# Performance work log

Hardware: AMD Instinct MI355X
Metric: run time of the kernel (lower is better)

## Reference

```python
import jax, jax.numpy as jnp
import numpy as np

VJ = 80                      # number of joints (groups)
DIMS = [480, 512, 256, 128, 64, 6]  # per-joint channel sizes through the 5 grouped 1x1 convs
RFF_K = 240                  # random fourier features -> 2*K = 480 channels
BATCH = 2048


def setup_inputs() -> dict:
    key = jax.random.key(0)
    ks = jax.random.split(key, 4 + 3 * 5)
    inp = {
        "querypoint": jax.random.normal(ks[0], (BATCH, VJ, 3), jnp.float32),
        "point_features": jax.random.normal(ks[1], (BATCH, VJ, DIMS[0]), jnp.float32),
        "adjmat": jax.random.uniform(ks[2], (VJ, VJ), jnp.float32),
        "Brff": jax.random.normal(ks[3], (3, RFF_K), jnp.float32),  # RandomFourierFeatEnc buffer (std=1)
    }
    ki = 4
    for i in range(5):
        cin, cout = DIMS[i], DIMS[i + 1]
        # weight_norm params: direction v [K, out, in], magnitude g [K, out], bias b [K, out]
        inp[f"v{i}"] = jax.random.normal(ks[ki], (VJ, cout, cin), jnp.float32) * 0.05; ki += 1
        inp[f"g{i}"] = jax.random.uniform(ks[ki], (VJ, cout), jnp.float32) + 0.5; ki += 1
        inp[f"b{i}"] = jax.random.normal(ks[ki], (VJ, cout), jnp.float32) * 0.01; ki += 1
    return inp


def _gconv(x, v, g, b):
    # grouped Conv1d(kernel=1, groups=VJ) == per-joint linear; weight_norm over per-output-channel fan-in
    w = v * (g / jnp.linalg.norm(v, axis=-1))[..., None]   # [K, out, in]
    return jnp.einsum('bki,koi->bko', x, w) + b            # [B, K, out]


def _leaky(x):
    return jnp.where(x >= 0, x, 0.01 * x)  # nn.LeakyReLU default slope


def reference(querypoint, point_features, adjmat, Brff,
              v0, g0, b0, v1, g1, b1, v2, g2, b2, v3, g3, b3, v4, g4, b4):
    # RandomFourierFeatEnc: cat(cos(2*pi*x@B), sin(2*pi*x@B))
    emb = 2.0 * jnp.pi * jnp.einsum('bnd,dk->bnk', querypoint, Brff)
    qf = jnp.concatenate([jnp.cos(emb), jnp.sin(emb)], axis=-1)   # [B, VJ, 480]
    h = point_features + qf
    # einsum 'bkjl,kk->bkjl' == scale each joint k by relu(adjmat)[k,k] (diagonal extraction)
    scale = jax.nn.relu(jnp.diagonal(adjmat))[None, :, None]      # [1, VJ, 1]
    h = _leaky(_gconv(h, v0, g0, b0)) * scale
    h = _leaky(_gconv(h, v1, g1, b1)) * scale
    h = _leaky(_gconv(h, v2, g2, b2)) * scale
    h = _leaky(_gconv(h, v3, g3, b3))
    return _gconv(h, v4, g4, b4)                                  # [B, VJ, 6]
```

## Files before the change

kernel.cpp:

```cpp
#include <hip/hip_runtime.h>
#include <hip/hip_fp16.h>

#define DI __device__ __forceinline__

typedef __attribute__((ext_vector_type(4))) float f32x4;
typedef __attribute__((ext_vector_type(8))) _Float16 f16x8;
typedef __attribute__((ext_vector_type(8))) short s16x8;

DI unsigned short f2h(float f) { return __half_as_ushort(__float2half(f)); }
DI float h2f(unsigned short u) { return __half2float(__ushort_as_half(u)); }

#define MFMA16(A, B, C) (C) = __builtin_amdgcn_mfma_f32_16x16x32_f16((A), (B), (C), 0, 0, 0)

struct PrepArgs {
    const float *adj;
    const float *v0,*g0,*b0,*v1,*g1,*b1,*v2,*g2,*b2,*v3,*g3,*b3,*v4,*g4,*b4;
    unsigned short *w0,*w1,*w2,*w3;
    float *w4, *bias0,*bias1,*bias2,*bias3,*bias4;
};

template <int CIN, int CINPAD>
DI void prep_row(const float* __restrict__ v, const float* __restrict__ g,
                 const float* __restrict__ b, const float* __restrict__ adj,
                 int cout, int use_scale,
                 unsigned short* __restrict__ wout, float* __restrict__ biasout,
                 int ridx, int lane)
{
    const int k = ridx / cout;
    const int o = ridx - k * cout;
    const float* vr = v + (size_t)ridx * CIN;
    float xv[8];
    if (lane * 8 < CIN) {
        const f32x4 p0 = *reinterpret_cast<const f32x4*>(&vr[lane * 8]);
        const f32x4 p1 = *reinterpret_cast<const f32x4*>(&vr[lane * 8 + 4]);
        #pragma unroll
        for (int e = 0; e < 4; e++) { xv[e] = p0[e]; xv[4 + e] = p1[e]; }
    } else {
        #pragma unroll
        for (int e = 0; e < 8; e++) xv[e] = 0.f;
    }
    float ss = 0.f;
    #pragma unroll
    for (int e = 0; e < 8; e++) ss += xv[e] * xv[e];
    #pragma unroll
    for (int off = 32; off >= 1; off >>= 1) ss += __shfl_xor(ss, off, 64);
    float s = g[ridx] / sqrtf(ss);
    float bias = b[ridx];
    if (use_scale) {
        float d = adj[k * 81];
        d = d > 0.f ? d : 0.f;
        s *= d; bias *= d;
    }
    if (lane == 0) biasout[ridx] = bias;
    if (lane < CINPAD / 8) {
        unsigned short tmp[8];
        #pragma unroll
        for (int e = 0; e < 8; e++) tmp[e] = f2h(xv[e] * s);
        unsigned short* wj = wout + (size_t)k * cout * CINPAD;
        const int sblk = lane >> 2, l4w = lane & 3;
        const size_t pos = (((size_t)sblk * (cout >> 4) + (o >> 4)) * 64 + l4w * 16 + (o & 15)) * 8;
        *reinterpret_cast<s16x8*>(&wj[pos]) = *reinterpret_cast<const s16x8*>(tmp);
    }
}

DI void prep_w4_row(const float* __restrict__ v, const float* __restrict__ g,
                    const float* __restrict__ b, float* __restrict__ wout,
                    float* __restrict__ biasout, int ridx, int lane)
{
    const float x = v[(size_t)ridx * 64 + lane];
    float ss = x * x;
    #pragma unroll
    for (int off = 32; off >= 1; off >>= 1) ss += __shfl_xor(ss, off, 64);
    const float s = g[ridx] / sqrtf(ss);
    if (lane == 0) biasout[ridx] = b[ridx];
    wout[(size_t)ridx * 64 + lane] = x * s;
}

__global__ __launch_bounds__(256) void prep_kernel(PrepArgs a)
{
    const int bid = blockIdx.x, wave = threadIdx.x >> 6, lane = threadIdx.x & 63;
    if (bid < 10240)      prep_row<480, 512>(a.v0, a.g0, a.b0, a.adj, 512, 1, a.w0, a.bias0, bid * 4 + wave, lane);
    else if (bid < 15360) prep_row<512, 512>(a.v1, a.g1, a.b1, a.adj, 256, 1, a.w1, a.bias1, (bid - 10240) * 4 + wave, lane);
    else if (bid < 17920) prep_row<256, 256>(a.v2, a.g2, a.b2, a.adj, 128, 1, a.w2, a.bias2, (bid - 15360) * 4 + wave, lane);
    else if (bid < 19200) prep_row<128, 128>(a.v3, a.g3, a.b3, a.adj,  64, 0, a.w3, a.bias3, (bid - 17920) * 4 + wave, lane);
    else                  prep_w4_row(a.v4, a.g4, a.b4, a.w4, a.bias4, (bid - 19200) * 4 + wave, lane);
}

struct MegaArgs {
    const float *qp, *pf, *Brff;
    const unsigned short *w0, *w1, *w2, *w3;
    const float *w4, *bias0, *bias1, *bias2, *bias3, *bias4;
    float* out;
};

__global__ __launch_bounds__(512, 4) void mega5_kernel(MegaArgs a)
{
    extern __shared__ __align__(16) unsigned short R0[];
    const int tid = threadIdx.x, wid = tid >> 6, lane = tid & 63;
    const int l15 = lane & 15, l4 = lane >> 4;
    const int bid = blockIdx.x;
    const int swz = (bid & 7) * 320 + (bid >> 3);
    const int kj = swz >> 5;
    const int m0 = (swz & 31) * 64;

    {
        const int row = tid >> 3;
        const int tq  = tid & 7;
        const int gr  = (m0 + row) * 80 + kj;
        const float q0 = a.qp[gr * 3 + 0], q1 = a.qp[gr * 3 + 1], q2 = a.qp[gr * 3 + 2];
        #pragma unroll
        for (int i = 0; i < 8; i++) {
            const int c0 = tq * 8 + i * 64;
            unsigned short o[8];
            if (c0 < 480) {
                const bool issin = (c0 >= 240);
                const int j0 = issin ? (c0 - 240) : c0;
                const f32x4 b0a = *reinterpret_cast<const f32x4*>(&a.Brff[j0]);
                const f32x4 b0b = *reinterpret_cast<const f32x4*>(&a.Brff[j0 + 4]);
                const f32x4 b1a = *reinterpret_cast<const f32x4*>(&a.Brff[240 + j0]);
                const f32x4 b1b = *reinterpret_cast<const f32x4*>(&a.Brff[240 + j0 + 4]);
                const f32x4 b2a = *reinterpret_cast<const f32x4*>(&a.Brff[480 + j0]);
                const f32x4 b2b = *reinterpret_cast<const f32x4*>(&a.Brff[480 + j0 + 4]);
                const f32x4 p0 = __builtin_nontemporal_load(
                    reinterpret_cast<const f32x4*>(&a.pf[(size_t)gr * 480 + c0]));
                const f32x4 p1 = __builtin_nontemporal_load(
                    reinterpret_cast<const f32x4*>(&a.pf[(size_t)gr * 480 + c0 + 4]));
                #pragma unroll
                for (int e = 0; e < 4; e++) {
                    float rev = q0 * b0a[e] + q1 * b1a[e] + q2 * b2a[e];
                    rev -= floorf(rev);
                    float t = issin ? __builtin_amdgcn_sinf(rev) : __builtin_amdgcn_cosf(rev);
                    o[e] = f2h(p0[e] + t);
                }
                #pragma unroll
                for (int e = 0; e < 4; e++) {
                    float rev = q0 * b0b[e] + q1 * b1b[e] + q2 * b2b[e];
                    rev -= floorf(rev);
                    float t = issin ? __builtin_amdgcn_sinf(rev) : __builtin_amdgcn_cosf(rev);
                    o[4 + e] = f2h(p1[e] + t);
                }
            } else {
                #pragma unroll
                for (int e = 0; e < 8; e++) o[e] = 0;
            }
            const int ck = c0 >> 3;
            *reinterpret_cast<s16x8*>(&R0[row * 512 + ((ck ^ (row & 7)) << 3)]) =
                *reinterpret_cast<const s16x8*>(o);
        }
    }
    __syncthreads();

    {
        const unsigned short* Wb = a.w0 + (size_t)kj * 262144 + (size_t)(wid * 4) * 512 + lane * 8;
        f32x4 acc[4][4] = {};
        f16x8 bfA[4], bfB[4];
        #pragma unroll
        for (int g = 0; g < 4; g++) bfA[g] = *reinterpret_cast<const f16x8*>(Wb + g * 512);
        #pragma unroll
        for (int ss = 0; ss < 8; ss++) {
            const int s0 = ss * 2, s1 = ss * 2 + 1;
            f16x8 af0[4];
            #pragma unroll
            for (int f = 0; f < 4; f++) {
                const int r = f * 16 + l15;
                af0[f] = *reinterpret_cast<const f16x8*>(&R0[r * 512 + (((s0 * 4 + l4) ^ (r & 7)) << 3)]);
            }
            #pragma unroll
            for (int g = 0; g < 4; g++)
                bfB[g] = *reinterpret_cast<const f16x8*>(Wb + (size_t)s1 * 16384 + g * 512);
            #pragma unroll
            for (int f = 0; f < 4; f++)
                #pragma unroll
                for (int g = 0; g < 4; g++)
                    MFMA16(af0[f], bfA[g], acc[f][g]);
            f16x8 af1[4];
            #pragma unroll
            for (int f = 0; f < 4; f++) {
                const int r = f * 16 + l15;
                af1[f] = *reinterpret_cast<const f16x8*>(&R0[r * 512 + (((s1 * 4 + l4) ^ (r & 7)) << 3)]);
            }
            if (ss < 7) {
                #pragma unroll
                for (int g = 0; g < 4; g++)
                    bfA[g] = *reinterpret_cast<const f16x8*>(Wb + (size_t)(s0 + 2) * 16384 + g * 512);
            }
            #pragma unroll
            for (int f = 0; f < 4; f++)
                #pragma unroll
                for (int g = 0; g < 4; g++)
                    MFMA16(af1[f], bfB[g], acc[f][g]);
        }
        __syncthreads();
        float bv[4];
        #pragma unroll
        for (int g = 0; g < 4; g++) bv[g] = a.bias0[kj * 512 + wid * 64 + g * 16 + l15];
        #pragma unroll
        for (int f = 0; f < 4; f++)
            #pragma unroll
            for (int g = 0; g < 4; g++)
                #pragma unroll
                for (int r = 0; r < 4; r++) {
                    float z = acc[f][g][r] + bv[g];
                    z = z >= 0.f ? z : 0.01f * z;
                    const int rr = f * 16 + l4 * 4 + r;
                    const int cc = wid * 64 + g * 16 + l15;
                    R0[rr * 512 + (((cc >> 3) ^ (rr & 7)) << 3) + (cc & 7)] = f2h(z);
                }
    }
    __syncthreads();

    {
        const unsigned short* Wb = a.w1 + (size_t)kj * 131072 + (size_t)(wid * 2) * 512 + lane * 8;
        f32x4 acc[4][2] = {};
        f16x8 bfA[2], bfB[2];
        #pragma unroll
        for (int g = 0; g < 2; g++) bfA[g] = *reinterpret_cast<const f16x8*>(Wb + g * 512);
        #pragma unroll
        for (int ss = 0; ss < 8; ss++) {
            const int s0 = ss * 2, s1 = ss * 2 + 1;
            f16x8 af0[4];
            #pragma unroll
            for (int f = 0; f < 4; f++) {
                const int r = f * 16 + l15;
                af0[f] = *reinterpret_cast<const f16x8*>(&R0[r * 512 + (((s0 * 4 + l4) ^ (r & 7)) << 3)]);
            }
            #pragma unroll
            for (int g = 0; g < 2; g++)
                bfB[g] = *reinterpret_cast<const f16x8*>(Wb + (size_t)s1 * 8192 + g * 512);
            #pragma unroll
            for (int f = 0; f < 4; f++)
                #pragma unroll
                for (int g = 0; g < 2; g++)
                    MFMA16(af0[f], bfA[g], acc[f][g]);
            f16x8 af1[4];
            #pragma unroll
            for (int f = 0; f < 4; f++) {
                const int r = f * 16 + l15;
                af1[f] = *reinterpret_cast<const f16x8*>(&R0[r * 512 + (((s1 * 4 + l4) ^ (r & 7)) << 3)]);
            }
            if (ss < 7) {
                #pragma unroll
                for (int g = 0; g < 2; g++)
                    bfA[g] = *reinterpret_cast<const f16x8*>(Wb + (size_t)(s0 + 2) * 8192 + g * 512);
            }
            #pragma unroll
            for (int f = 0; f < 4; f++)
                #pragma unroll
                for (int g = 0; g < 2; g++)
                    MFMA16(af1[f], bfB[g], acc[f][g]);
        }
        __syncthreads();
        float bv[2];
        #pragma unroll
        for (int g = 0; g < 2; g++) bv[g] = a.bias1[kj * 256 + wid * 32 + g * 16 + l15];
        #pragma unroll
        for (int f = 0; f < 4; f++)
            #pragma unroll
            for (int g = 0; g < 2; g++)
                #pragma unroll
                for (int r = 0; r < 4; r++) {
                    float z = acc[f][g][r] + bv[g];
                    z = z >= 0.f ? z : 0.01f * z;
                    const int rr = f * 16 + l4 * 4 + r;
                    const int cc = wid * 32 + g * 16 + l15;
                    R0[rr * 256 + (((cc >> 3) ^ (rr & 7)) << 3) + (cc & 7)] = f2h(z);
                }
    }
    __syncthreads();

    {
        const unsigned short* Wb = a.w2 + (size_t)kj * 32768 + (size_t)wid * 512 + lane * 8;
        f32x4 acc[4] = {};
        f16x8 bfA, bfB;
        bfA = *reinterpret_cast<const f16x8*>(Wb);
        #pragma unroll
        for (int ss = 0; ss < 4; ss++) {
            const int s0 = ss * 2, s1 = ss * 2 + 1;
            f16x8 af0[4];
            #pragma unroll
            for (int f = 0; f < 4; f++) {
                const int r = f * 16 + l15;
                af0[f] = *reinterpret_cast<const f16x8*>(&R0[r * 256 + (((s0 * 4 + l4) ^ (r & 7)) << 3)]);
            }
            bfB = *reinterpret_cast<const f16x8*>(Wb + (size_t)s1 * 4096);
            #pragma unroll
            for (int f = 0; f < 4; f++)
                MFMA16(af0[f], bfA, acc[f]);
            f16x8 af1[4];
            #pragma unroll
            for (int f = 0; f < 4; f++) {
                const int r = f * 16 + l15;
                af1[f] = *reinterpret_cast<const f16x8*>(&R0[r * 256 + (((s1 * 4 + l4) ^ (r & 7)) << 3)]);
            }
            if (ss < 3) bfA = *reinterpret_cast<const f16x8*>(Wb + (size_t)(s0 + 2) * 4096);
            #pragma unroll
            for (int f = 0; f < 4; f++)
                MFMA16(af1[f], bfB, acc[f]);
        }
        __syncthreads();
        const float bv = a.bias2[kj * 128 + wid * 16 + l15];
        #pragma unroll
        for (int f = 0; f < 4; f++)
            #pragma unroll
            for (int r = 0; r < 4; r++) {
                float z = acc[f][r] + bv;
                z = z >= 0.f ? z : 0.01f * z;
                const int rr = f * 16 + l4 * 4 + r;
                const int cc = wid * 16 + l15;
                R0[rr * 128 + (((cc >> 3) ^ (rr & 7)) << 3) + (cc & 7)] = f2h(z);
            }
    }
    __syncthreads();

    {
        const int wm = wid >> 2, wn4 = wid & 3;
        const unsigned short* Wb = a.w3 + (size_t)kj * 8192 + (size_t)wn4 * 512 + lane * 8;
        f32x4 acc[2] = {};
        #pragma unroll
        for (int s = 0; s < 4; s++) {
            f16x8 af[2], bf;
            #pragma unroll
            for (int f = 0; f < 2; f++) {
                const int r = wm * 32 + f * 16 + l15;
                af[f] = *reinterpret_cast<const f16x8*>(&R0[r * 128 + (((s * 4 + l4) ^ (r & 7)) << 3)]);
            }
            bf = *reinterpret_cast<const f16x8*>(Wb + (size_t)s * 2048);
            #pragma unroll
            for (int f = 0; f < 2; f++)
                MFMA16(af[f], bf, acc[f]);
        }
        __syncthreads();
        const float bv = a.bias3[kj * 64 + wn4 * 16 + l15];
        #pragma unroll
        for (int f = 0; f < 2; f++)
            #pragma unroll
            for (int r = 0; r < 4; r++) {
                float z = acc[f][r] + bv;
                z = z >= 0.f ? z : 0.01f * z;
                const int rr = wm * 32 + f * 16 + l4 * 4 + r;
                const int cc = wn4 * 16 + l15;
                R0[rr * 64 + (((cc >> 3) ^ (rr & 7)) << 3) + (cc & 7)] = f2h(z);
            }
    }
    __syncthreads();

    if (tid < 64) {
        const int row = tid;
        float xv[64];
        #pragma unroll
        for (int ch = 0; ch < 8; ch++) {
            s16x8 v = *reinterpret_cast<const s16x8*>(&R0[row * 64 + ((ch ^ (row & 7)) << 3)]);
            #pragma unroll
            for (int e = 0; e < 8; e++) xv[ch * 8 + e] = h2f((unsigned short)v[e]);
        }
        const float* w4b = a.w4 + kj * 384;
        float* op = a.out + ((size_t)(m0 + row) * 80 + kj) * 6;
        #pragma unroll
        for (int o = 0; o < 6; o++) {
            float sum = a.bias4[kj * 6 + o];
            #pragma unroll
            for (int i = 0; i < 64; i++) sum = fmaf(xv[i], w4b[o * 64 + i], sum);
            __builtin_nontemporal_store(sum, &op[o]);
        }
    }
}

extern "C" void kernel_launch(void* const* d_in, const int* in_sizes, int n_in,
                              void* d_out, int out_size, void* d_ws, size_t ws_size,
                              hipStream_t stream)
{
    (void)in_sizes; (void)n_in; (void)out_size; (void)ws_size;
    PrepArgs a;
    a.adj  = (const float*)d_in[2];
    a.v0 = (const float*)d_in[4];  a.g0 = (const float*)d_in[5];  a.b0 = (const float*)d_in[6];
    a.v1 = (const float*)d_in[7];  a.g1 = (const float*)d_in[8];  a.b1 = (const float*)d_in[9];
    a.v2 = (const float*)d_in[10]; a.g2 = (const float*)d_in[11]; a.b2 = (const float*)d_in[12];
    a.v3 = (const float*)d_in[13]; a.g3 = (const float*)d_in[14]; a.b3 = (const float*)d_in[15];
    a.v4 = (const float*)d_in[16]; a.g4 = (const float*)d_in[17]; a.b4 = (const float*)d_in[18];

    char* ws = (char*)d_ws;
    size_t off = 0;
    auto alloc = [&](size_t n) -> void* {
        off = (off + 255) & ~(size_t)255;
        void* p = ws + off;
        off += n;
        return p;
    };
    a.w0 = (unsigned short*)alloc(80ull * 512 * 512 * 2);
    a.w1 = (unsigned short*)alloc(80ull * 256 * 512 * 2);
    a.w2 = (unsigned short*)alloc(80ull * 128 * 256 * 2);
    a.w3 = (unsigned short*)alloc(80ull * 64 * 128 * 2);
    a.w4 = (float*)alloc(80ull * 6 * 64 * 4);
    a.bias0 = (float*)alloc(80ull * 512 * 4);
    a.bias1 = (float*)alloc(80ull * 256 * 4);
    a.bias2 = (float*)alloc(80ull * 128 * 4);
    a.bias3 = (float*)alloc(80ull * 64 * 4);
    a.bias4 = (float*)alloc(80ull * 6 * 4);

    MegaArgs m;
    m.qp   = (const float*)d_in[0];
    m.pf   = (const float*)d_in[1];
    m.Brff = (const float*)d_in[3];
    m.w0 = a.w0; m.w1 = a.w1; m.w2 = a.w2; m.w3 = a.w3; m.w4 = a.w4;
    m.bias0 = a.bias0; m.bias1 = a.bias1; m.bias2 = a.bias2;
    m.bias3 = a.bias3; m.bias4 = a.bias4;
    m.out = (float*)d_out;

    (void)hipFuncSetAttribute((const void*)mega5_kernel,
                              hipFuncAttributeMaxDynamicSharedMemorySize, 65536);

    prep_kernel<<<19320, 256, 0, stream>>>(a);
    mega5_kernel<<<2560, 512, 65536, stream>>>(m);
}
```

Measured before the change: 283.3 us.

## Replace XOR-swizzled LDS layout with padded rows and parallelize final layer

The activation buffer in shared memory switches from an XOR-swizzled layout, whose row stride shrinks each layer, to a fixed padded row stride of 520 halves for every layer. This simplifies address computation and is meant to avoid bank conflicts through padding. The RFF stage now computes cos and sin from one projection per thread, halving the Fourier projection math. The final 64->6 layer is spread over 384 threads, one output each, instead of 64 threads doing six outputs. Shared memory per block grows from 64 KiB to 65 KiB, which could reduce occupancy, and the padding may leave bank conflicts on some access patterns.

```diff
diff --git a/kernel.cpp b/kernel.cpp
--- a/kernel.cpp
+++ b/kernel.cpp
@@ -93,7 +93,9 @@
     float* out;
 };
 
-__global__ __launch_bounds__(512, 4) void mega5_kernel(MegaArgs a)
+constexpr int LDP = 520;
+
+__global__ __launch_bounds__(512, 4) void mega6_kernel(MegaArgs a)
 {
     extern __shared__ __align__(16) unsigned short R0[];
     const int tid = threadIdx.x, wid = tid >> 6, lane = tid & 63;
@@ -104,51 +106,56 @@
     const int m0 = (swz & 31) * 64;
 
     {
-        const int row = tid >> 3;
-        const int tq  = tid & 7;
-        const int gr  = (m0 + row) * 80 + kj;
+        const int row = tid >> 3, tq = tid & 7;
+        const int gr = (m0 + row) * 80 + kj;
         const float q0 = a.qp[gr * 3 + 0], q1 = a.qp[gr * 3 + 1], q2 = a.qp[gr * 3 + 2];
         #pragma unroll
-        for (int i = 0; i < 8; i++) {
-            const int c0 = tq * 8 + i * 64;
-            unsigned short o[8];
-            if (c0 < 480) {
-                const bool issin = (c0 >= 240);
-                const int j0 = issin ? (c0 - 240) : c0;
-                const f32x4 b0a = *reinterpret_cast<const f32x4*>(&a.Brff[j0]);
-                const f32x4 b0b = *reinterpret_cast<const f32x4*>(&a.Brff[j0 + 4]);
-                const f32x4 b1a = *reinterpret_cast<const f32x4*>(&a.Brff[240 + j0]);
-                const f32x4 b1b = *reinterpret_cast<const f32x4*>(&a.Brff[240 + j0 + 4]);
-                const f32x4 b2a = *reinterpret_cast<const f32x4*>(&a.Brff[480 + j0]);
-                const f32x4 b2b = *reinterpret_cast<const f32x4*>(&a.Brff[480 + j0 + 4]);
-                const f32x4 p0 = __builtin_nontemporal_load(
+        for (int i = 0; i < 4; i++) {
+            const int jc = tq + i * 8;
+            if (jc < 30) {
+                const int c0 = jc * 8;
+                const f32x4 b0a = *reinterpret_cast<const f32x4*>(&a.Brff[c0]);
+                const f32x4 b0b = *reinterpret_cast<const f32x4*>(&a.Brff[c0 + 4]);
+                const f32x4 b1a = *reinterpret_cast<const f32x4*>(&a.Brff[240 + c0]);
+                const f32x4 b1b = *reinterpret_cast<const f32x4*>(&a.Brff[240 + c0 + 4]);
+                const f32x4 b2a = *reinterpret_cast<const f32x4*>(&a.Brff[480 + c0]);
+                const f32x4 b2b = *reinterpret_cast<const f32x4*>(&a.Brff[480 + c0 + 4]);
+                const f32x4 pc0 = __builtin_nontemporal_load(
                     reinterpret_cast<const f32x4*>(&a.pf[(size_t)gr * 480 + c0]));
-                const f32x4 p1 = __builtin_nontemporal_load(
+                const f32x4 pc1 = __builtin_nontemporal_load(
                     reinterpret_cast<const f32x4*>(&a.pf[(size_t)gr * 480 + c0 + 4]));
+                const f32x4 ps0 = __builtin_nontemporal_load(
+                    reinterpret_cast<const f32x4*>(&a.pf[(size_t)gr * 480 + c0 + 240]));
+                const f32x4 ps1 = __builtin_nontemporal_load(
+                    reinterpret_cast<const f32x4*>(&a.pf[(size_t)gr * 480 + c0 + 244]));
+                unsigned short oc[8], os[8];
                 #pragma unroll
                 for (int e = 0; e < 4; e++) {
                     float rev = q0 * b0a[e] + q1 * b1a[e] + q2 * b2a[e];
                     rev -= floorf(rev);
-                    float t = issin ? __builtin_amdgcn_sinf(rev) : __builtin_amdgcn_cosf(rev);
-                    o[e] = f2h(p0[e] + t);
+                    oc[e] = f2h(pc0[e] + __builtin_amdgcn_cosf(rev));
+                    os[e] = f2h(ps0[e] + __builtin_amdgcn_sinf(rev));
                 }
                 #pragma unroll
                 for (int e = 0; e < 4; e++) {
                     float rev = q0 * b0b[e] + q1 * b1b[e] + q2 * b2b[e];
                     rev -= floorf(rev);
-                    float t = issin ? __builtin_amdgcn_sinf(rev) : __builtin_amdgcn_cosf(rev);
-                    o[4 + e] = f2h(p1[e] + t);
+                    oc[4 + e] = f2h(pc1[e] + __builtin_amdgcn_cosf(rev));
+                    os[4 + e] = f2h(ps1[e] + __builtin_amdgcn_sinf(rev));
                 }
+                *reinterpret_cast<s16x8*>(&R0[row * LDP + c0]) = *reinterpret_cast<const s16x8*>(oc);
+                *reinterpret_cast<s16x8*>(&R0[row * LDP + c0 + 240]) = *reinterpret_cast<const s16x8*>(os);
             } else {
-                #pragma unroll
-                for (int e = 0; e < 8; e++) o[e] = 0;
+                const s16x8 z = {0, 0, 0, 0, 0, 0, 0, 0};
+                const int c0 = 480 + (jc - 30) * 16;
+                *reinterpret_cast<s16x8*>(&R0[row * LDP + c0]) = z;
+                *reinterpret_cast<s16x8*>(&R0[row * LDP + c0 + 8]) = z;
             }
-            const int ck = c0 >> 3;
-            *reinterpret_cast<s16x8*>(&R0[row * 512 + ((ck ^ (row & 7)) << 3)]) =
-                *reinterpret_cast<const s16x8*>(o);
         }
     }
     __syncthreads();
+
+    const int abase = l15 * LDP + l4 * 8;
 
     {
         const unsigned short* Wb = a.w0 + (size_t)kj * 262144 + (size_t)(wid * 4) * 512 + lane * 8;
@@ -161,10 +168,8 @@
             const int s0 = ss * 2, s1 = ss * 2 + 1;
             f16x8 af0[4];
             #pragma unroll
-            for (int f = 0; f < 4; f++) {
-                const int r = f * 16 + l15;
-                af0[f] = *reinterpret_cast<const f16x8*>(&R0[r * 512 + (((s0 * 4 + l4) ^ (r & 7)) << 3)]);
-            }
+            for (int f = 0; f < 4; f++)
+                af0[f] = *reinterpret_cast<const f16x8*>(&R0[abase + f * 16 * LDP + s0 * 32]);
             #pragma unroll
             for (int g = 0; g < 4; g++)
                 bfB[g] = *reinterpret_cast<const f16x8*>(Wb + (size_t)s1 * 16384 + g * 512);
@@ -175,10 +180,8 @@
                     MFMA16(af0[f], bfA[g], acc[f][g]);
             f16x8 af1[4];
             #pragma unroll
-            for (int f = 0; f < 4; f++) {
-                const int r = f * 16 + l15;
-                af1[f] = *reinterpret_cast<const f16x8*>(&R0[r * 512 + (((s1 * 4 + l4) ^ (r & 7)) << 3)]);
-            }
+            for (int f = 0; f < 4; f++)
+                af1[f] = *reinterpret_cast<const f16x8*>(&R0[abase + f * 16 * LDP + s1 * 32]);
             if (ss < 7) {
                 #pragma unroll
                 for (int g = 0; g < 4; g++)
@@ -194,6 +197,7 @@
         float bv[4];
         #pragma unroll
         for (int g = 0; g < 4; g++) bv[g] = a.bias0[kj * 512 + wid * 64 + g * 16 + l15];
+        const int wb = (l4 * 4) * LDP + wid * 64 + l15;
         #pragma unroll
         for (int f = 0; f < 4; f++)
             #pragma unroll
@@ -202,9 +206,7 @@
                 for (int r = 0; r < 4; r++) {
                     float z = acc[f][g][r] + bv[g];
                     z = z >= 0.f ? z : 0.01f * z;
-                    const int rr = f * 16 + l4 * 4 + r;
-                    const int cc = wid * 64 + g * 16 + l15;
-                    R0[rr * 512 + (((cc >> 3) ^ (rr & 7)) << 3) + (cc & 7)] = f2h(z);
+                    R0[wb + (f * 16 + r) * LDP + g * 16] = f2h(z);
                 }
     }
     __syncthreads();
@@ -220,10 +222,8 @@
             const int s0 = ss * 2, s1 = ss * 2 + 1;
             f16x8 af0[4];
             #pragma unroll
-            for (int f = 0; f < 4; f++) {
-                const int r = f * 16 + l15;
-                af0[f] = *reinterpret_cast<const f16x8*>(&R0[r * 512 + (((s0 * 4 + l4) ^ (r & 7)) << 3)]);
-            }
+            for (int f = 0; f < 4; f++)
+                af0[f] = *reinterpret_cast<const f16x8*>(&R0[abase + f * 16 * LDP + s0 * 32]);
             #pragma unroll
             for (int g = 0; g < 2; g++)
                 bfB[g] = *reinterpret_cast<const f16x8*>(Wb + (size_t)s1 * 8192 + g * 512);
@@ -234,10 +234,8 @@
                     MFMA16(af0[f], bfA[g], acc[f][g]);
             f16x8 af1[4];
             #pragma unroll
-            for (int f = 0; f < 4; f++) {
-                const int r = f * 16 + l15;
-                af1[f] = *reinterpret_cast<const f16x8*>(&R0[r * 512 + (((s1 * 4 + l4) ^ (r & 7)) << 3)]);
-            }
+            for (int f = 0; f < 4; f++)
+                af1[f] = *reinterpret_cast<const f16x8*>(&R0[abase + f * 16 * LDP + s1 * 32]);
             if (ss < 7) {
                 #pragma unroll
                 for (int g = 0; g < 2; g++)
@@ -253,6 +251,7 @@
         float bv[2];
         #pragma unroll
         for (int g = 0; g < 2; g++) bv[g] = a.bias1[kj * 256 + wid * 32 + g * 16 + l15];
+        const int wb = (l4 * 4) * LDP + wid * 32 + l15;
         #pragma unroll
         for (int f = 0; f < 4; f++)
             #pragma unroll
@@ -261,9 +260,7 @@
                 for (int r = 0; r < 4; r++) {
                     float z = acc[f][g][r] + bv[g];
                     z = z >= 0.f ? z : 0.01f * z;
-                    const int rr = f * 16 + l4 * 4 + r;
-                    const int cc = wid * 32 + g * 16 + l15;
-                    R0[rr * 256 + (((cc >> 3) ^ (rr & 7)) << 3) + (cc & 7)] = f2h(z);
+                    R0[wb + (f * 16 + r) * LDP + g * 16] = f2h(z);
                 }
     }
     __syncthreads();
@@ -278,20 +275,16 @@
             const int s0 = ss * 2, s1 = ss * 2 + 1;
             f16x8 af0[4];
             #pragma unroll
-            for (int f = 0; f < 4; f++) {
-                const int r = f * 16 + l15;
-                af0[f] = *reinterpret_cast<const f16x8*>(&R0[r * 256 + (((s0 * 4 + l4) ^ (r & 7)) << 3)]);
-            }
+            for (int f = 0; f < 4; f++)
+                af0[f] = *reinterpret_cast<const f16x8*>(&R0[abase + f * 16 * LDP + s0 * 32]);
             bfB = *reinterpret_cast<const f16x8*>(Wb + (size_t)s1 * 4096);
             #pragma unroll
             for (int f = 0; f < 4; f++)
                 MFMA16(af0[f], bfA, acc[f]);
             f16x8 af1[4];
             #pragma unroll
-            for (int f = 0; f < 4; f++) {
-                const int r = f * 16 + l15;
-                af1[f] = *reinterpret_cast<const f16x8*>(&R0[r * 256 + (((s1 * 4 + l4) ^ (r & 7)) << 3)]);
-            }
+            for (int f = 0; f < 4; f++)
+                af1[f] = *reinterpret_cast<const f16x8*>(&R0[abase + f * 16 * LDP + s1 * 32]);
             if (ss < 3) bfA = *reinterpret_cast<const f16x8*>(Wb + (size_t)(s0 + 2) * 4096);
             #pragma unroll
             for (int f = 0; f < 4; f++)
@@ -299,15 +292,14 @@
         }
         __syncthreads();
         const float bv = a.bias2[kj * 128 + wid * 16 + l15];
+        const int wb = (l4 * 4) * LDP + wid * 16 + l15;
         #pragma unroll
         for (int f = 0; f < 4; f++)
             #pragma unroll
             for (int r = 0; r < 4; r++) {
                 float z = acc[f][r] + bv;
                 z = z >= 0.f ? z : 0.01f * z;
-                const int rr = f * 16 + l4 * 4 + r;
-                const int cc = wid * 16 + l15;
-                R0[rr * 128 + (((cc >> 3) ^ (rr & 7)) << 3) + (cc & 7)] = f2h(z);
+                R0[wb + (f * 16 + r) * LDP] = f2h(z);
             }
     }
     __syncthreads();
@@ -315,15 +307,14 @@
     {
         const int wm = wid >> 2, wn4 = wid & 3;
         const unsigned short* Wb = a.w3 + (size_t)kj * 8192 + (size_t)wn4 * 512 + lane * 8;
+        const int abase3 = (wm * 32 + l15) * LDP + l4 * 8;
         f32x4 acc[2] = {};
         #pragma unroll
         for (int s = 0; s < 4; s++) {
             f16x8 af[2], bf;
             #pragma unroll
-            for (int f = 0; f < 2; f++) {
-                const int r = wm * 32 + f * 16 + l15;
-                af[f] = *reinterpret_cast<const f16x8*>(&R0[r * 128 + (((s * 4 + l4) ^ (r & 7)) << 3)]);
-            }
+            for (int f = 0; f < 2; f++)
+                af[f] = *reinterpret_cast<const f16x8*>(&R0[abase3 + f * 16 * LDP + s * 32]);
             bf = *reinterpret_cast<const f16x8*>(Wb + (size_t)s * 2048);
             #pragma unroll
             for (int f = 0; f < 2; f++)
@@ -331,37 +322,32 @@
         }
         __syncthreads();
         const float bv = a.bias3[kj * 64 + wn4 * 16 + l15];
+        const int wb = (wm * 32 + l4 * 4) * LDP + wn4 * 16 + l15;
         #pragma unroll
         for (int f = 0; f < 2; f++)
             #pragma unroll
             for (int r = 0; r < 4; r++) {
                 float z = acc[f][r] + bv;
                 z = z >= 0.f ? z : 0.01f * z;
-                const int rr = wm * 32 + f * 16 + l4 * 4 + r;
-                const int cc = wn4 * 16 + l15;
-                R0[rr * 64 + (((cc >> 3) ^ (rr & 7)) << 3) + (cc & 7)] = f2h(z);
+                R0[wb + (f * 16 + r) * LDP] = f2h(z);
             }
     }
     __syncthreads();
 
-    if (tid < 64) {
-        const int row = tid;
+    if (tid < 384) {
+        const int row = tid / 6, o = tid - row * 6;
         float xv[64];
         #pragma unroll
         for (int ch = 0; ch < 8; ch++) {
-            s16x8 v = *reinterpret_cast<const s16x8*>(&R0[row * 64 + ((ch ^ (row & 7)) << 3)]);
+            s16x8 v = *reinterpret_cast<const s16x8*>(&R0[row * LDP + ch * 8]);
             #pragma unroll
             for (int e = 0; e < 8; e++) xv[ch * 8 + e] = h2f((unsigned short)v[e]);
         }
-        const float* w4b = a.w4 + kj * 384;
-        float* op = a.out + ((size_t)(m0 + row) * 80 + kj) * 6;
-        #pragma unroll
-        for (int o = 0; o < 6; o++) {
-            float sum = a.bias4[kj * 6 + o];
-            #pragma unroll
-            for (int i = 0; i < 64; i++) sum = fmaf(xv[i], w4b[o * 64 + i], sum);
-            __builtin_nontemporal_store(sum, &op[o]);
-        }
+        const float* w4b = a.w4 + kj * 384 + o * 64;
+        float sum = a.bias4[kj * 6 + o];
+        #pragma unroll
+        for (int i = 0; i < 64; i++) sum = fmaf(xv[i], w4b[i], sum);
+        __builtin_nontemporal_store(sum, &a.out[((size_t)(m0 + row) * 80 + kj) * 6 + o]);
     }
 }
 
@@ -406,9 +392,9 @@
     m.bias3 = a.bias3; m.bias4 = a.bias4;
     m.out = (float*)d_out;
 
-    (void)hipFuncSetAttribute((const void*)mega5_kernel,
-                              hipFuncAttributeMaxDynamicSharedMemorySize, 65536);
+    (void)hipFuncSetAttribute((const void*)mega6_kernel,
+                              hipFuncAttributeMaxDynamicSharedMemorySize, 66560);
 
     prep_kernel<<<19320, 256, 0, stream>>>(a);
-    mega5_kernel<<<2560, 512, 65536, stream>>>(m);
+    mega6_kernel<<<2560, 512, 66560, stream>>>(m);
 }
```

Measured after the change: 322.9 us. 14.0% more time.

## Raise MFMA wave priority, trim padded K-step, parallelize final projection

Applied to the files above, without the earlier changes.

Wraps MFMA bursts in s_setprio so matrix-issuing waves get priority over waves doing memory loads. Drops the zero-padded K-step in layer 0 by peeling the last step and skipping zero LDS writes for the padding columns. Spreads the final 64-to-6 projection over 384 threads, one per output, instead of 64 threads each computing six outputs. This adds redundant LDS reads of each row, and the priority change may perturb scheduling.

```diff
diff --git a/kernel.cpp b/kernel.cpp
--- a/kernel.cpp
+++ b/kernel.cpp
@@ -11,6 +11,8 @@
 DI float h2f(unsigned short u) { return __half2float(__ushort_as_half(u)); }
 
 #define MFMA16(A, B, C) (C) = __builtin_amdgcn_mfma_f32_16x16x32_f16((A), (B), (C), 0, 0, 0)
+#define PRIO1 __builtin_amdgcn_s_setprio(1)
+#define PRIO0 __builtin_amdgcn_s_setprio(0)
 
 struct PrepArgs {
     const float *adj;
@@ -93,7 +95,7 @@
     float* out;
 };
 
-__global__ __launch_bounds__(512, 4) void mega5_kernel(MegaArgs a)
+__global__ __launch_bounds__(512, 4) void mega7_kernel(MegaArgs a)
 {
     extern __shared__ __align__(16) unsigned short R0[];
     const int tid = threadIdx.x, wid = tid >> 6, lane = tid & 63;
@@ -111,8 +113,8 @@
         #pragma unroll
         for (int i = 0; i < 8; i++) {
             const int c0 = tq * 8 + i * 64;
-            unsigned short o[8];
             if (c0 < 480) {
+                unsigned short o[8];
                 const bool issin = (c0 >= 240);
                 const int j0 = issin ? (c0 - 240) : c0;
                 const f32x4 b0a = *reinterpret_cast<const f32x4*>(&a.Brff[j0]);
@@ -139,13 +141,10 @@
                     float t = issin ? __builtin_amdgcn_sinf(rev) : __builtin_amdgcn_cosf(rev);
                     o[4 + e] = f2h(p1[e] + t);
                 }
-            } else {
-                #pragma unroll
-                for (int e = 0; e < 8; e++) o[e] = 0;
-            }
-            const int ck = c0 >> 3;
-            *reinterpret_cast<s16x8*>(&R0[row * 512 + ((ck ^ (row & 7)) << 3)]) =
-                *reinterpret_cast<const s16x8*>(o);
+                const int ck = c0 >> 3;
+                *reinterpret_cast<s16x8*>(&R0[row * 512 + ((ck ^ (row & 7)) << 3)]) =
+                    *reinterpret_cast<const s16x8*>(o);
+            }
         }
     }
     __syncthreads();
@@ -157,7 +156,7 @@
         #pragma unroll
         for (int g = 0; g < 4; g++) bfA[g] = *reinterpret_cast<const f16x8*>(Wb + g * 512);
         #pragma unroll
-        for (int ss = 0; ss < 8; ss++) {
+        for (int ss = 0; ss < 7; ss++) {
             const int s0 = ss * 2, s1 = ss * 2 + 1;
             f16x8 af0[4];
             #pragma unroll
@@ -168,27 +167,44 @@
             #pragma unroll
             for (int g = 0; g < 4; g++)
                 bfB[g] = *reinterpret_cast<const f16x8*>(Wb + (size_t)s1 * 16384 + g * 512);
+            PRIO1;
             #pragma unroll
             for (int f = 0; f < 4; f++)
                 #pragma unroll
                 for (int g = 0; g < 4; g++)
                     MFMA16(af0[f], bfA[g], acc[f][g]);
+            PRIO0;
             f16x8 af1[4];
             #pragma unroll
             for (int f = 0; f < 4; f++) {
                 const int r = f * 16 + l15;
                 af1[f] = *reinterpret_cast<const f16x8*>(&R0[r * 512 + (((s1 * 4 + l4) ^ (r & 7)) << 3)]);
             }
-            if (ss < 7) {
-                #pragma unroll
-                for (int g = 0; g < 4; g++)
-                    bfA[g] = *reinterpret_cast<const f16x8*>(Wb + (size_t)(s0 + 2) * 16384 + g * 512);
-            }
+            #pragma unroll
+            for (int g = 0; g < 4; g++)
+                bfA[g] = *reinterpret_cast<const f16x8*>(Wb + (size_t)(s0 + 2) * 16384 + g * 512);
+            PRIO1;
             #pragma unroll
             for (int f = 0; f < 4; f++)
                 #pragma unroll
                 for (int g = 0; g < 4; g++)
                     MFMA16(af1[f], bfB[g], acc[f][g]);
+            PRIO0;
+        }
+        {
+            f16x8 af0[4];
+            #pragma unroll
+            for (int f = 0; f < 4; f++) {
+                const int r = f * 16 + l15;
+                af0[f] = *reinterpret_cast<const f16x8*>(&R0[r * 512 + (((14 * 4 + l4) ^ (r & 7)) << 3)]);
+            }
+            PRIO1;
+            #pragma unroll
+            for (int f = 0; f < 4; f++)
+                #pragma unroll
+                for (int g = 0; g < 4; g++)
+                    MFMA16(af0[f], bfA[g], acc[f][g]);
+            PRIO0;
         }
         __syncthreads();
         float bv[4];
@@ -227,11 +243,13 @@
             #pragma unroll
             for (int g = 0; g < 2; g++)
                 bfB[g] = *reinterpret_cast<const f16x8*>(Wb + (size_t)s1 * 8192 + g * 512);
+            PRIO1;
             #pragma unroll
             for (int f = 0; f < 4; f++)
                 #pragma unroll
                 for (int g = 0; g < 2; g++)
                     MFMA16(af0[f], bfA[g], acc[f][g]);
+            PRIO0;
             f16x8 af1[4];
             #pragma unroll
             for (int f = 0; f < 4; f++) {
@@ -243,11 +261,13 @@
                 for (int g = 0; g < 2; g++)
                     bfA[g] = *reinterpret_cast<const f16x8*>(Wb + (size_t)(s0 + 2) * 8192 + g * 512);
             }
+            PRIO1;
             #pragma unroll
             for (int f = 0; f < 4; f++)
                 #pragma unroll
                 for (int g = 0; g < 2; g++)
                     MFMA16(af1[f], bfB[g], acc[f][g]);
+            PRIO0;
         }
         __syncthreads();
         float bv[2];
@@ -283,9 +303,11 @@
                 af0[f] = *reinterpret_cast<const f16x8*>(&R0[r * 256 + (((s0 * 4 + l4) ^ (r & 7)) << 3)]);
             }
             bfB = *reinterpret_cast<const f16x8*>(Wb + (size_t)s1 * 4096);
+            PRIO1;
             #pragma unroll
             for (int f = 0; f < 4; f++)
                 MFMA16(af0[f], bfA, acc[f]);
+            PRIO0;
             f16x8 af1[4];
             #pragma unroll
             for (int f = 0; f < 4; f++) {
@@ -293,9 +315,11 @@
                 af1[f] = *reinterpret_cast<const f16x8*>(&R0[r * 256 + (((s1 * 4 + l4) ^ (r & 7)) << 3)]);
             }
             if (ss < 3) bfA = *reinterpret_cast<const f16x8*>(Wb + (size_t)(s0 + 2) * 4096);
+            PRIO1;
             #pragma unroll
             for (int f = 0; f < 4; f++)
                 MFMA16(af1[f], bfB, acc[f]);
+            PRIO0;
         }
         __syncthreads();
         const float bv = a.bias2[kj * 128 + wid * 16 + l15];
@@ -325,9 +349,11 @@
                 af[f] = *reinterpret_cast<const f16x8*>(&R0[r * 128 + (((s * 4 + l4) ^ (r & 7)) << 3)]);
             }
             bf = *reinterpret_cast<const f16x8*>(Wb + (size_t)s * 2048);
+            PRIO1;
             #pragma unroll
             for (int f = 0; f < 2; f++)
                 MFMA16(af[f], bf, acc[f]);
+            PRIO0;
         }
         __syncthreads();
         const float bv = a.bias3[kj * 64 + wn4 * 16 + l15];
@@ -344,8 +370,8 @@
     }
     __syncthreads();
 
-    if (tid < 64) {
-        const int row = tid;
+    if (tid < 384) {
+        const int row = tid / 6, o = tid - row * 6;
         float xv[64];
         #pragma unroll
         for (int ch = 0; ch < 8; ch++) {
@@ -353,15 +379,11 @@
             #pragma unroll
             for (int e = 0; e < 8; e++) xv[ch * 8 + e] = h2f((unsigned short)v[e]);
         }
-        const float* w4b = a.w4 + kj * 384;
-        float* op = a.out + ((size_t)(m0 + row) * 80 + kj) * 6;
-        #pragma unroll
-        for (int o = 0; o < 6; o++) {
-            float sum = a.bias4[kj * 6 + o];
-            #pragma unroll
-            for (int i = 0; i < 64; i++) sum = fmaf(xv[i], w4b[o * 64 + i], sum);
-            __builtin_nontemporal_store(sum, &op[o]);
-        }
+        const float* w4b = a.w4 + kj * 384 + o * 64;
+        float sum = a.bias4[kj * 6 + o];
+        #pragma unroll
+        for (int i = 0; i < 64; i++) sum = fmaf(xv[i], w4b[i], sum);
+        __builtin_nontemporal_store(sum, &a.out[((size_t)(m0 + row) * 80 + kj) * 6 + o]);
     }
 }
 
@@ -406,9 +428,9 @@
     m.bias3 = a.bias3; m.bias4 = a.bias4;
     m.out = (float*)d_out;
 
-    (void)hipFuncSetAttribute((const void*)mega5_kernel,
+    (void)hipFuncSetAttribute((const void*)mega7_kernel,
                               hipFuncAttributeMaxDynamicSharedMemorySize, 65536);
 
     prep_kernel<<<19320, 256, 0, stream>>>(a);
-    mega5_kernel<<<2560, 512, 65536, stream>>>(m);
+    mega7_kernel<<<2560, 512, 65536, stream>>>(m);
 }
```

Measured after the change: 311.1 us. 9.8% more time.
